# Performance work log

Measured on AMD Instinct MI355X. Metric: run time of the kernel, lower is better.

## Reference

```python
import jax, jax.numpy as jnp
import numpy as np

B, N, C_ATT, H, L = 4, 2048, 256, 8, 2
TOPK = 32        # torch.topk k (only index 0 per channel is used)
NSAMPLE = 32     # max_radius_points
RADIUS = 0.3
EPS = 1e-5


def _bn(x, g, b, axes):
    # training-mode batch norm (biased variance), channel dim = 1
    m = jnp.mean(x, axes, keepdims=True)
    v = jnp.var(x, axes, keepdims=True)
    sh = [1] * x.ndim
    sh[1] = -1
    return (x - m) / jnp.sqrt(v + EPS) * g.reshape(sh) + b.reshape(sh)


def _ln(x, g, b):
    m = jnp.mean(x, -1, keepdims=True)
    v = jnp.var(x, -1, keepdims=True)
    return (x - m) / jnp.sqrt(v + EPS) * g + b


def setup_inputs() -> dict:
    key = jax.random.key(0)
    ks = iter(jax.random.split(key, 40))
    def w(shape, fan):
        return jax.random.normal(next(ks), shape, jnp.float32) / np.sqrt(fan)
    return {
        "hoch_features": jax.random.normal(next(ks), (B, C_ATT, N), jnp.float32),
        "pts": jax.random.uniform(next(ks), (B, 3, N), jnp.float32),
        "Wq": w((L, C_ATT, C_ATT), C_ATT), "Wk": w((L, C_ATT, C_ATT), C_ATT),
        "Wv": w((L, C_ATT, C_ATT), C_ATT), "Wo": w((L, C_ATT, C_ATT), C_ATT),
        "ln_g": jnp.ones((L, C_ATT)), "ln_b": jnp.zeros((L, C_ATT)),
        "fg_w1": w((64, C_ATT), C_ATT), "fg_b1": jnp.zeros((64,)),
        "fg_w2": w((32, 64), 64), "fg_b2": jnp.zeros((32,)),
        "fg_w3": w((16, 32), 32), "fg_b3": jnp.zeros((16,)),
        "fg_g1": jnp.ones((64,)), "fg_be1": jnp.zeros((64,)),
        "fg_g2": jnp.ones((32,)), "fg_be2": jnp.zeros((32,)),
        "fg_g3": jnp.ones((16,)), "fg_be3": jnp.zeros((16,)),
        "cw1": w((64, 3), 3), "cw2": w((256, 64), 64), "cw3": w((512, 256), 256),
        "cg1": jnp.ones((64,)), "cb1": jnp.zeros((64,)),
        "cg2": jnp.ones((256,)), "cb2": jnp.zeros((256,)),
        "cg3": jnp.ones((512,)), "cb3": jnp.zeros((512,)),
    }


def _forward(hoch_features, pts, Wq, Wk, Wv, Wo, ln_g, ln_b,
             fg_w1, fg_b1, fg_w2, fg_b2, fg_w3, fg_b3,
             fg_g1, fg_be1, fg_g2, fg_be2, fg_g3, fg_be3,
             cw1, cw2, cw3, cg1, cb1, cg2, cb2, cg3, cb3):
    # ---- multi-head self-attention stack on (B,N,C) ----
    x = hoch_features.transpose(0, 2, 1)
    dh = C_ATT // H
    for l in range(L):
        q = (x @ Wq[l]).reshape(B, N, H, dh)
        k = (x @ Wk[l]).reshape(B, N, H, dh)
        v = (x @ Wv[l]).reshape(B, N, H, dh)
        att = jax.nn.softmax(jnp.einsum('bnhd,bmhd->bhnm', q, k) / np.sqrt(dh).astype(np.float32))
        o = jnp.einsum('bhnm,bmhd->bnhd', att, v).reshape(B, N, C_ATT) @ Wo[l]
        x = _ln(x + o, ln_g[l], ln_b[l])
    feats = x.transpose(0, 2, 1)                      # (B,256,N)
    # ---- feat_generator: 1x1 conv1d -> BN -> relu chain 256->64->32->16 ----
    h = jax.nn.relu(_bn(jnp.einsum('oc,bcn->bon', fg_w1, feats) + fg_b1[:, None], fg_g1, fg_be1, (0, 2)))
    h = jax.nn.relu(_bn(jnp.einsum('oc,bcn->bon', fg_w2, h) + fg_b2[:, None], fg_g2, fg_be2, (0, 2)))
    h = jax.nn.relu(_bn(jnp.einsum('oc,bcn->bon', fg_w3, h) + fg_b3[:, None], fg_g3, fg_be3, (0, 2)))  # (B,16,N)
    # ---- topk over points, keep argmax per channel -> 16 query points ----
    _, ti = jax.lax.top_k(h, TOPK)                    # (B,16,32)
    idx = ti[:, :, 0]                                 # (B,16)
    all_pts = pts.transpose(0, 2, 1)                  # (B,N,3)
    qpts = jax.vmap(lambda p, i: p[i])(all_pts, idx)  # (B,16,3)
    # ---- ball query (fixed-radius kNN fill, PointNet++ style) ----
    sqd = (jnp.sum(qpts * qpts, -1)[:, :, None] + jnp.sum(all_pts * all_pts, -1)[:, None, :]
           - 2.0 * jnp.einsum('bsc,bnc->bsn', qpts, all_pts))      # (B,16,N)
    gi = jnp.broadcast_to(jnp.arange(N), sqd.shape)
    gi = jnp.where(sqd > RADIUS * RADIUS, N, gi)
    gi = jnp.sort(gi, axis=-1)[:, :, :NSAMPLE]
    gi = jnp.where(gi == N, gi[:, :, :1], gi)         # (B,16,32)
    rpts = jax.vmap(lambda p, i: p[i])(all_pts, gi)   # (B,16,32,3)
    grouped = jnp.concatenate([qpts[:, :, None, :], rpts], axis=2)  # (B,16,33,3)
    g = grouped.transpose(0, 3, 1, 2)                 # (B,3,16,33)
    # ---- 1x1 conv2d -> BN2d -> LeakyReLU(0.2) chain 3->64->256->512 ----
    lrelu = lambda t: jnp.where(t > 0, t, 0.2 * t)
    g = lrelu(_bn(jnp.einsum('oc,bcsk->bosk', cw1, g), cg1, cb1, (0, 2, 3)))
    g = lrelu(_bn(jnp.einsum('oc,bcsk->bosk', cw2, g), cg2, cb2, (0, 2, 3)))
    g = lrelu(_bn(jnp.einsum('oc,bcsk->bosk', cw3, g), cg3, cb3, (0, 2, 3)))
    return jnp.max(g, axis=-1)                        # (B,512,16)


def reference(hoch_features, pts, Wq, Wk, Wv, Wo, ln_g, ln_b,
              fg_w1, fg_b1, fg_w2, fg_b2, fg_w3, fg_b3,
              fg_g1, fg_be1, fg_g2, fg_be2, fg_g3, fg_be3,
              cw1, cw2, cw3, cg1, cb1, cg2, cb2, cg3, cb3):
    return _forward(hoch_features, pts, Wq, Wk, Wv, Wo, ln_g, ln_b,
                    fg_w1, fg_b1, fg_w2, fg_b2, fg_w3, fg_b3,
                    fg_g1, fg_be1, fg_g2, fg_be2, fg_g3, fg_be3,
                    cw1, cw2, cw3, cg1, cb1, cg2, cb2, cg3, cb3)
```

## Files before the change

### kernel.cpp

```cpp
#include <hip/hip_runtime.h>
#include <hip/hip_bf16.h>
#include <math.h>

#define BB 4
#define NN 2048
#define CC 256
#define HH 8
#define DH 32
#define LL 2
#define SS 16
#define KK 33
#define NSAMPLE 32
#define EPSV 1e-5f

typedef _Float16 f16x8 __attribute__((ext_vector_type(8)));
typedef _Float16 f16x4 __attribute__((ext_vector_type(4)));
typedef float f32x4 __attribute__((ext_vector_type(4)));

struct hl16 { _Float16 h, l; };
__device__ __forceinline__ hl16 split2(float v) {
    hl16 r;
    r.h = (_Float16)v;
    r.l = (_Float16)(v - (float)r.h);
    return r;
}

#define INV_MF (1.f / 8192.f)
#define INV_MG (1.f / 2112.f)

#define WT_SLOT 65536
#define FG1H_OFF 1048576
#define FG1L_OFF (FG1H_OFF + 16384)
#define CW2H_OFF (FG1H_OFF + 32768)
#define CW2L_OFF (FG1H_OFF + 49152)
#define CW3H_OFF (FG1H_OFF + 65536)
#define CW3L_OFF (CW3H_OFF + 131072)

__global__ __launch_bounds__(256) void prep_split_k(
    const float* __restrict__ Wq, const float* __restrict__ Wk,
    const float* __restrict__ Wv, const float* __restrict__ Wo,
    const float* __restrict__ fgw1, const float* __restrict__ cw2,
    const float* __restrict__ cw3, _Float16* __restrict__ wt,
    float* __restrict__ stats0) {
    int e = blockIdx.x * 256 + threadIdx.x;
    if (e < 6144) stats0[e] = 0.f;
    if (e < 524288) {
        int slot = e >> 16;
        int l = slot >> 2, mat = slot & 3;
        int r = e & 65535;
        int n = r >> 8, k = r & 255;
        const float* W = mat == 0 ? Wq : mat == 1 ? Wk : mat == 2 ? Wv : Wo;
        hl16 s = split2(W[(size_t)l * 65536 + k * 256 + n]);
        wt[(size_t)(2 * slot) * WT_SLOT + n * 256 + k] = s.h;
        wt[(size_t)(2 * slot + 1) * WT_SLOT + n * 256 + k] = s.l;
    } else if (e < 524288 + 16384) {
        int r = e - 524288;
        hl16 s = split2(fgw1[r]);
        wt[FG1H_OFF + r] = s.h;
        wt[FG1L_OFF + r] = s.l;
    } else if (e < 524288 + 32768) {
        int r = e - (524288 + 16384);
        hl16 s = split2(cw2[r]);
        wt[CW2H_OFF + r] = s.h;
        wt[CW2L_OFF + r] = s.l;
    } else if (e < 524288 + 32768 + 131072) {
        int r = e - (524288 + 32768);
        hl16 s = split2(cw3[r]);
        wt[CW3H_OFF + r] = s.h;
        wt[CW3L_OFF + r] = s.l;
    }
}

__global__ __launch_bounds__(256) void transpose_split_k(const float* __restrict__ in,
                                                         float* __restrict__ out,
                                                         _Float16* __restrict__ oh,
                                                         _Float16* __restrict__ ol) {
    __shared__ float tls[32][33];
    int n0 = blockIdx.x * 32, c0 = blockIdx.y * 32, b = blockIdx.z;
    const float* ip = in + (size_t)b * CC * NN;
    size_t ob = (size_t)b * NN * CC;
    int tx = threadIdx.x, ty = threadIdx.y;
#pragma unroll
    for (int i = 0; i < 4; ++i)
        tls[ty + i * 8][tx] = ip[(size_t)(c0 + ty + i * 8) * NN + n0 + tx];
    __syncthreads();
#pragma unroll
    for (int i = 0; i < 4; ++i) {
        size_t oi = ob + (size_t)(n0 + ty + i * 8) * CC + c0 + tx;
        float v = tls[tx][ty + i * 8];
        out[oi] = v;
        hl16 s = split2(v);
        oh[oi] = s.h;
        ol[oi] = s.l;
    }
}

template <bool TRANSB, bool BIAS>
__global__ __launch_bounds__(256) void gemm_k(const float* __restrict__ A,
                                              const float* __restrict__ Bm,
                                              const float* __restrict__ bias,
                                              float* __restrict__ Cm,
                                              int M, int Nc, int K,
                                              const float* __restrict__ pst,
                                              const float* __restrict__ pg,
                                              const float* __restrict__ pb,
                                              float pInvM,
                                              float* __restrict__ ost) {
    __shared__ float As[16][68];
    __shared__ float Bs[16][68];
    __shared__ float sSc[64], sSh[64];
    int t = threadIdx.x;
    int tx = t & 15, ty = t >> 4;
    int row0 = blockIdx.y * 64, col0 = blockIdx.x * 64;
    if (pst && t < K) {
        float mean = pst[t] * pInvM;
        float var = pst[K + t] * pInvM - mean * mean;
        float wv = rsqrtf(var + EPSV) * pg[t];
        sSc[t] = wv;
        sSh[t] = pb[t] - mean * wv;
    }
    if (pst) __syncthreads();
    float acc[4][4] = {};
    for (int k0 = 0; k0 < K; k0 += 16) {
#pragma unroll
        for (int p = 0; p < 4; ++p) {
            int i = t + 256 * p;
            int m = i >> 4, k = i & 15;
            int gm = row0 + m, gk = k0 + k;
            float av = 0.f;
            if (gm < M && gk < K) {
                av = A[(size_t)gm * K + gk];
                if (pst) {
                    av = fmaf(av, sSc[gk], sSh[gk]);
                    av = fmaxf(av, 0.f);
                }
            }
            As[k][m] = av;
        }
#pragma unroll
        for (int p = 0; p < 4; ++p) {
            int i = t + 256 * p;
            if (TRANSB) {
                int k = i & 15, n = i >> 4;
                int gn = col0 + n, gk = k0 + k;
                Bs[k][n] = (gn < Nc && gk < K) ? Bm[(size_t)gn * K + gk] : 0.f;
            } else {
                int n = i & 63, k = i >> 6;
                int gn = col0 + n, gk = k0 + k;
                Bs[k][n] = (gn < Nc && gk < K) ? Bm[(size_t)gk * Nc + gn] : 0.f;
            }
        }
        __syncthreads();
#pragma unroll
        for (int kk = 0; kk < 16; ++kk) {
            float4 a4 = *(const float4*)&As[kk][ty * 4];
            float4 b4 = *(const float4*)&Bs[kk][tx * 4];
            float av[4] = {a4.x, a4.y, a4.z, a4.w};
            float bv[4] = {b4.x, b4.y, b4.z, b4.w};
#pragma unroll
            for (int i = 0; i < 4; ++i)
#pragma unroll
                for (int j = 0; j < 4; ++j) acc[i][j] = fmaf(av[i], bv[j], acc[i][j]);
        }
        __syncthreads();
    }
    float cs[4] = {}, css[4] = {};
#pragma unroll
    for (int i = 0; i < 4; ++i) {
        int r = row0 + ty * 4 + i;
        if (r >= M) continue;
#pragma unroll
        for (int j = 0; j < 4; ++j) {
            int c = col0 + tx * 4 + j;
            if (c >= Nc) continue;
            float v = acc[i][j];
            if (BIAS) v += bias[c];
            Cm[(size_t)r * Nc + c] = v;
            cs[j] += v;
            css[j] += v * v;
        }
    }
    if (ost) {
        float* sc = &As[0][0];
        if (t < 128) sc[t] = 0.f;
        __syncthreads();
#pragma unroll
        for (int j = 0; j < 4; ++j) {
            atomicAdd(&sc[tx * 4 + j], cs[j]);
            atomicAdd(&sc[64 + tx * 4 + j], css[j]);
        }
        __syncthreads();
        if (t < Nc) atomicAdd(&ost[t], sc[t]);
        else if (t >= 64 && t - 64 < Nc) atomicAdd(&ost[Nc + t - 64], sc[t]);
    }
}

#define EPI_F32 0
#define EPI_QK 1
#define EPI_VT 2

template <int TM>
__device__ __forceinline__ void gemm_h_body(
    const _Float16* __restrict__ Ah, const _Float16* __restrict__ Al,
    const _Float16* __restrict__ Bh, const _Float16* __restrict__ Bl,
    const float* __restrict__ bias, float* __restrict__ Cf,
    _Float16* __restrict__ Ch, _Float16* __restrict__ Cl,
    int Nc, int K, int row0, int col0, int mode, float scl,
    float* __restrict__ ost,
    _Float16* sAh, _Float16* sAl, _Float16* sBh, _Float16* sBl) {
    int t = threadIdx.x, w = t >> 6, lane = t & 63;
    int col = lane & 15, quad = lane >> 4;
    const int m0w = (TM == 128) ? (w & 1) * 64 : 0;
    const int n0w = (TM == 128) ? (w >> 1) * 32 : w * 16;
    constexpr int NT = (TM == 128) ? 2 : 1;
    constexpr int AC = TM / 64;
    f32x4 acc[4][NT];
#pragma unroll
    for (int i = 0; i < 4; ++i)
#pragma unroll
        for (int j = 0; j < NT; ++j) acc[i][j] = (f32x4){0.f, 0.f, 0.f, 0.f};

    for (int k0 = 0; k0 < K; k0 += 32) {
        f16x8 rah[AC], ral[AC], rbh, rbl;
#pragma unroll
        for (int i = 0; i < AC; ++i) {
            int idx = t + 256 * i;
            int r = idx >> 2, off = (idx & 3) * 8;
            rah[i] = *(const f16x8*)(Ah + (size_t)(row0 + r) * K + k0 + off);
            ral[i] = *(const f16x8*)(Al + (size_t)(row0 + r) * K + k0 + off);
        }
        {
            int r = t >> 2, off = (t & 3) * 8;
            rbh = *(const f16x8*)(Bh + (size_t)(col0 + r) * K + k0 + off);
            rbl = *(const f16x8*)(Bl + (size_t)(col0 + r) * K + k0 + off);
        }
        __syncthreads();
#pragma unroll
        for (int i = 0; i < AC; ++i) {
            int idx = t + 256 * i;
            int r = idx >> 2, off = (idx & 3) * 8;
            *(f16x8*)&sAh[r * 40 + off] = rah[i];
            *(f16x8*)&sAl[r * 40 + off] = ral[i];
        }
        {
            int r = t >> 2, off = (t & 3) * 8;
            *(f16x8*)&sBh[r * 40 + off] = rbh;
            *(f16x8*)&sBl[r * 40 + off] = rbl;
        }
        __syncthreads();
        f16x8 fah[4], fal[4], fbh[NT], fbl[NT];
#pragma unroll
        for (int i = 0; i < 4; ++i) {
            fah[i] = *(const f16x8*)&sAh[(m0w + i * 16 + col) * 40 + quad * 8];
            fal[i] = *(const f16x8*)&sAl[(m0w + i * 16 + col) * 40 + quad * 8];
        }
#pragma unroll
        for (int j = 0; j < NT; ++j) {
            fbh[j] = *(const f16x8*)&sBh[(n0w + j * 16 + col) * 40 + quad * 8];
            fbl[j] = *(const f16x8*)&sBl[(n0w + j * 16 + col) * 40 + quad * 8];
        }
#pragma unroll
        for (int i = 0; i < 4; ++i)
#pragma unroll
            for (int j = 0; j < NT; ++j) {
                acc[i][j] = __builtin_amdgcn_mfma_f32_16x16x32_f16(fah[i], fbh[j], acc[i][j], 0, 0, 0);
                acc[i][j] = __builtin_amdgcn_mfma_f32_16x16x32_f16(fah[i], fbl[j], acc[i][j], 0, 0, 0);
                acc[i][j] = __builtin_amdgcn_mfma_f32_16x16x32_f16(fal[i], fbh[j], acc[i][j], 0, 0, 0);
            }
    }
    float s = 0.f, ss = 0.f;
#pragma unroll
    for (int i = 0; i < 4; ++i)
#pragma unroll
        for (int j = 0; j < NT; ++j) {
            int n = col0 + n0w + j * 16 + col;
            int mb = row0 + m0w + i * 16 + quad * 4;
            if (mode == EPI_F32) {
                float bv = bias ? bias[n] : 0.f;
#pragma unroll
                for (int r = 0; r < 4; ++r) {
                    float v = acc[i][j][r] + bv;
                    Cf[(size_t)(mb + r) * Nc + n] = v;
                    s += v;
                    ss += v * v;
                }
            } else if (mode == EPI_QK) {
#pragma unroll
                for (int r = 0; r < 4; ++r) {
                    hl16 sp = split2(acc[i][j][r] * scl);
                    Ch[(size_t)(mb + r) * Nc + n] = sp.h;
                    Cl[(size_t)(mb + r) * Nc + n] = sp.l;
                }
            } else {
                int b = mb >> 11, token = mb & 2047;
                int h = n >> 5, d = n & 31;
                f16x4 h4, l4;
#pragma unroll
                for (int r = 0; r < 4; ++r) {
                    hl16 sp = split2(acc[i][j][r]);
                    h4[r] = sp.h;
                    l4[r] = sp.l;
                }
                size_t dst = ((size_t)(b * HH + h) * DH + d) * NN + token;
                *(f16x4*)&Ch[dst] = h4;
                *(f16x4*)&Cl[dst] = l4;
            }
        }
    if (ost && mode == EPI_F32 && TM == 64) {
        s += __shfl_xor(s, 16);
        s += __shfl_xor(s, 32);
        ss += __shfl_xor(ss, 16);
        ss += __shfl_xor(ss, 32);
        if (quad == 0) {
            int n = col0 + n0w + col;
            atomicAdd(&ost[n], s);
            atomicAdd(&ost[Nc + n], ss);
        }
    }
}

template <int TM>
__global__ __launch_bounds__(256) void gemm_h_k(const _Float16* __restrict__ Ah,
                                                const _Float16* __restrict__ Al,
                                                const _Float16* __restrict__ Bh,
                                                const _Float16* __restrict__ Bl,
                                                const float* __restrict__ bias,
                                                float* __restrict__ Cf, int Nc, int K,
                                                float* __restrict__ ost) {
    __shared__ _Float16 sAh[TM * 40], sAl[TM * 40], sBh[64 * 40], sBl[64 * 40];
    gemm_h_body<TM>(Ah, Al, Bh, Bl, bias, Cf, nullptr, nullptr, Nc, K,
                    blockIdx.y * TM, blockIdx.x * 64, EPI_F32, 1.f, ost,
                    sAh, sAl, sBh, sBl);
}

__global__ __launch_bounds__(256) void qkv_h_k(const _Float16* __restrict__ Xh,
                                               const _Float16* __restrict__ Xl,
                                               const _Float16* __restrict__ wt, int layer,
                                               _Float16* Qh, _Float16* Ql,
                                               _Float16* Kh, _Float16* Kl,
                                               _Float16* Vh, _Float16* Vl) {
    __shared__ _Float16 sAh[128 * 40], sAl[128 * 40], sBh[64 * 40], sBl[64 * 40];
    int mat = blockIdx.x >> 2;
    int slot = (layer * 4 + mat) * 2;
    const _Float16* Bh = wt + (size_t)slot * WT_SLOT;
    const _Float16* Bl = wt + (size_t)(slot + 1) * WT_SLOT;
    _Float16* Ch = mat == 0 ? Qh : mat == 1 ? Kh : Vh;
    _Float16* Cl = mat == 0 ? Ql : mat == 1 ? Kl : Vl;
    int mode = (mat == 2) ? EPI_VT : EPI_QK;
    float scl = (mat == 0) ? 0.25501654859214384f : 1.f;
    gemm_h_body<128>(Xh, Xl, Bh, Bl, nullptr, nullptr, Ch, Cl, CC, CC,
                     blockIdx.y * 128, (blockIdx.x & 3) * 64, mode, scl, nullptr,
                     sAh, sAl, sBh, sBl);
}

__global__ __launch_bounds__(256) void attn5_k(_Float16* QOh, _Float16* QOl,
                                               const _Float16* __restrict__ Kh,
                                               const _Float16* __restrict__ Kl,
                                               const _Float16* __restrict__ Vh,
                                               const _Float16* __restrict__ Vl) {
    __shared__ _Float16 sKh[64 * 40], sKl[64 * 40];
    __shared__ _Float16 sVh[32 * 72], sVl[32 * 72];
    __shared__ _Float16 sPh[4][16 * 40], sPl[4][16 * 40];
    int t = threadIdx.x, w = t >> 6, lane = t & 63;
    int col = lane & 15, quad = lane >> 4;
    int bh = blockIdx.y, b = bh >> 3, h = bh & 7;
    int qbase = blockIdx.x * 64 + w * 16;

    size_t qoff = ((size_t)(b * NN + qbase + col)) * CC + h * DH + quad * 8;
    f16x8 qh = *(const f16x8*)(QOh + qoff);
    f16x8 ql = *(const f16x8*)(QOl + qoff);

    f32x4 o0 = {0.f, 0.f, 0.f, 0.f}, o1 = {0.f, 0.f, 0.f, 0.f};
    float mrun = -1e30f, lsum = 0.f;

    const _Float16* fKh = &sKh[col * 40 + quad * 8];
    const _Float16* fKl = &sKl[col * 40 + quad * 8];
    const _Float16* fVh0 = &sVh[col * 72 + quad * 8];
    const _Float16* fVl0 = &sVl[col * 72 + quad * 8];
    const _Float16* fVh1 = &sVh[(16 + col) * 72 + quad * 8];
    const _Float16* fVl1 = &sVl[(16 + col) * 72 + quad * 8];
    _Float16* wPh = &sPh[w][col * 40 + quad * 4];
    _Float16* wPl = &sPl[w][col * 40 + quad * 4];
    const _Float16* rPh = &sPh[w][col * 40 + quad * 8];
    const _Float16* rPl = &sPl[w][col * 40 + quad * 8];

    int pidx = t & 127;
    int krow = pidx >> 1, koff = (pidx & 1) * 16;
    int vrow = pidx >> 2, voff = (pidx & 3) * 16;
    const _Float16* kg = (t < 128 ? Kh : Kl) + (size_t)b * NN * CC + h * DH;
    const _Float16* vg = (t < 128 ? Vh : Vl) + ((size_t)(b * HH + h) * DH + vrow) * NN;
    _Float16* dK = (t < 128 ? sKh : sKl) + krow * 40 + koff;
    _Float16* dV = (t < 128 ? sVh : sVl) + vrow * 72 + voff;

    for (int k0 = 0; k0 < NN; k0 += 64) {
        const _Float16* kp = kg + (size_t)(k0 + krow) * CC + koff;
        f16x8 rk0 = *(const f16x8*)kp;
        f16x8 rk1 = *(const f16x8*)(kp + 8);
        const _Float16* vp = vg + k0 + voff;
        f16x8 rv0 = *(const f16x8*)vp;
        f16x8 rv1 = *(const f16x8*)(vp + 8);
        __syncthreads();
        *(f16x8*)dK = rk0;
        *(f16x8*)(dK + 8) = rk1;
        *(f16x8*)dV = rv0;
        *(f16x8*)(dV + 8) = rv1;
        __syncthreads();

        f32x4 s[4];
#pragma unroll
        for (int kt = 0; kt < 4; ++kt) {
            f16x8 ka = *(const f16x8*)(fKh + kt * 16 * 40);
            f16x8 kb = *(const f16x8*)(fKl + kt * 16 * 40);
            f32x4 z = {0.f, 0.f, 0.f, 0.f};
            z = __builtin_amdgcn_mfma_f32_16x16x32_f16(ka, qh, z, 0, 0, 0);
            z = __builtin_amdgcn_mfma_f32_16x16x32_f16(ka, ql, z, 0, 0, 0);
            z = __builtin_amdgcn_mfma_f32_16x16x32_f16(kb, qh, z, 0, 0, 0);
            s[kt] = z;
        }

        float tm = -1e30f;
#pragma unroll
        for (int kt = 0; kt < 4; ++kt)
#pragma unroll
            for (int r = 0; r < 4; ++r) tm = fmaxf(tm, s[kt][r]);
        tm = fmaxf(tm, __shfl_xor(tm, 16));
        tm = fmaxf(tm, __shfl_xor(tm, 32));
        float nm = fmaxf(mrun, tm);
        float alpha = __builtin_amdgcn_exp2f(mrun - nm);
        float p[16], rs = 0.f;
#pragma unroll
        for (int kt = 0; kt < 4; ++kt)
#pragma unroll
            for (int r = 0; r < 4; ++r) {
                float pv = __builtin_amdgcn_exp2f(s[kt][r] - nm);
                p[kt * 4 + r] = pv;
                rs += pv;
            }
        rs += __shfl_xor(rs, 16);
        rs += __shfl_xor(rs, 32);
        lsum = lsum * alpha + rs;
        mrun = nm;
        o0.x *= alpha; o0.y *= alpha; o0.z *= alpha; o0.w *= alpha;
        o1.x *= alpha; o1.y *= alpha; o1.z *= alpha; o1.w *= alpha;

#pragma unroll
        for (int c = 0; c < 2; ++c) {
#pragma unroll
            for (int k2 = 0; k2 < 2; ++k2) {
                int kt = c * 2 + k2;
                f16x4 h4, l4;
#pragma unroll
                for (int r = 0; r < 4; ++r) {
                    hl16 sp = split2(p[kt * 4 + r]);
                    h4[r] = sp.h;
                    l4[r] = sp.l;
                }
                *(f16x4*)(wPh + k2 * 16) = h4;
                *(f16x4*)(wPl + k2 * 16) = l4;
            }
            __asm__ volatile("s_waitcnt lgkmcnt(0)" ::: "memory");
            f16x8 pH = *(const f16x8*)rPh;
            f16x8 pL = *(const f16x8*)rPl;

            f16x8 va = *(const f16x8*)(fVh0 + c * 32);
            f16x8 vb = *(const f16x8*)(fVl0 + c * 32);
            o0 = __builtin_amdgcn_mfma_f32_16x16x32_f16(va, pH, o0, 0, 0, 0);
            o0 = __builtin_amdgcn_mfma_f32_16x16x32_f16(va, pL, o0, 0, 0, 0);
            o0 = __builtin_amdgcn_mfma_f32_16x16x32_f16(vb, pH, o0, 0, 0, 0);
            f16x8 vc = *(const f16x8*)(fVh1 + c * 32);
            f16x8 vd = *(const f16x8*)(fVl1 + c * 32);
            o1 = __builtin_amdgcn_mfma_f32_16x16x32_f16(vc, pH, o1, 0, 0, 0);
            o1 = __builtin_amdgcn_mfma_f32_16x16x32_f16(vc, pL, o1, 0, 0, 0);
            o1 = __builtin_amdgcn_mfma_f32_16x16x32_f16(vd, pH, o1, 0, 0, 0);
        }
    }

    float inv = 1.f / lsum;
    f32x4 oo[2] = {o0, o1};
#pragma unroll
    for (int dh = 0; dh < 2; ++dh) {
        f16x4 h4, l4;
#pragma unroll
        for (int r = 0; r < 4; ++r) {
            hl16 s = split2(oo[dh][r] * inv);
            h4[r] = s.h;
            l4[r] = s.l;
        }
        size_t dsti = ((size_t)(b * NN + qbase + col)) * CC + h * DH + dh * 16 + quad * 4;
        *(f16x4*)&QOh[dsti] = h4;
        *(f16x4*)&QOl[dsti] = l4;
    }
}

__global__ __launch_bounds__(256) void add_ln_k(float* __restrict__ X,
                                                const float* __restrict__ P,
                                                const float* __restrict__ g,
                                                const float* __restrict__ bta,
                                                _Float16* __restrict__ Xh,
                                                _Float16* __restrict__ Xl) {
    int wave = threadIdx.x >> 6, lane = threadIdx.x & 63;
    size_t row = (size_t)blockIdx.x * 4 + wave;
    size_t base = row * CC + lane * 4;
    float4 x = *(float4*)(X + base);
    float4 p = *(const float4*)(P + base);
    x.x += p.x; x.y += p.y; x.z += p.z; x.w += p.w;
    float sum = x.x + x.y + x.z + x.w;
    float ss = x.x * x.x + x.y * x.y + x.z * x.z + x.w * x.w;
#pragma unroll
    for (int off = 32; off; off >>= 1) {
        sum += __shfl_down(sum, off);
        ss += __shfl_down(ss, off);
    }
    sum = __shfl(sum, 0);
    ss = __shfl(ss, 0);
    float mean = sum * (1.f / 256.f);
    float var = ss * (1.f / 256.f) - mean * mean;
    float wn = rsqrtf(var + EPSV);
    float4 gg = *(const float4*)(g + lane * 4);
    float4 bb = *(const float4*)(bta + lane * 4);
    x.x = (x.x - mean) * wn * gg.x + bb.x;
    x.y = (x.y - mean) * wn * gg.y + bb.y;
    x.z = (x.z - mean) * wn * gg.z + bb.z;
    x.w = (x.w - mean) * wn * gg.w + bb.w;
    *(float4*)(X + base) = x;
    f16x4 h4, l4;
    float xv[4] = {x.x, x.y, x.z, x.w};
#pragma unroll
    for (int j = 0; j < 4; ++j) {
        hl16 s = split2(xv[j]);
        h4[j] = s.h;
        l4[j] = s.l;
    }
    *(f16x4*)&Xh[base] = h4;
    *(f16x4*)&Xl[base] = l4;
}

__global__ __launch_bounds__(256) void applyc_k(const float* __restrict__ in,
                                                _Float16* __restrict__ oh,
                                                _Float16* __restrict__ ol,
                                                const float* __restrict__ st,
                                                const float* __restrict__ gam,
                                                const float* __restrict__ bet,
                                                int total, int Cc, float invM) {
    int i = blockIdx.x * 256 + threadIdx.x;
    if (i >= total) return;
    int c = i % Cc;
    float mean = st[c] * invM;
    float var = st[Cc + c] * invM - mean * mean;
    float sc = rsqrtf(var + EPSV) * gam[c];
    float v = fmaf(in[i] - mean, sc, bet[c]);
    v = v > 0.f ? v : 0.2f * v;
    hl16 s = split2(v);
    oh[i] = s.h;
    ol[i] = s.l;
}

__global__ __launch_bounds__(64) void select_k(const float* __restrict__ H3,
                                               const float* __restrict__ pts,
                                               const float* __restrict__ st,
                                               const float* __restrict__ gam,
                                               const float* __restrict__ bet,
                                               float* __restrict__ G0) {
    int bs = blockIdx.x;
    int b = bs >> 4, ch = bs & 15;
    int lane = threadIdx.x;
    float mean = st[ch] * INV_MF;
    float var = st[16 + ch] * INV_MF - mean * mean;
    float sc = rsqrtf(var + EPSV) * gam[ch];
    float sh = bet[ch] - mean * sc;
    float best = -1e30f;
    int bn = 0;
    for (int n = lane; n < NN; n += 64) {
        float v = fmaf(H3[((size_t)(b * NN + n)) * 16 + ch], sc, sh);
        v = fmaxf(v, 0.f);
        if (v > best) { best = v; bn = n; }
    }
#pragma unroll
    for (int off = 32; off; off >>= 1) {
        float ov = __shfl_xor(best, off);
        int on = __shfl_xor(bn, off);
        if (ov > best || (ov == best && on < bn)) { best = ov; bn = on; }
    }
    const float* px = pts + (size_t)b * 3 * NN;
    float qx = px[bn], qy = px[NN + bn], qz = px[2 * NN + bn];
    float qq = (qx * qx + qy * qy) + qz * qz;
    __shared__ int sgi[NSAMPLE];
    const float R2 = 0.09f;
    int cnt = 0;
    for (int base = 0; base < NN && cnt < NSAMPLE; base += 64) {
        int n = base + lane;
        float x = px[n], y = px[NN + n], z = px[2 * NN + n];
        float pp = (x * x + y * y) + z * z;
        float dot = (qx * x + qy * y) + qz * z;
        float sqd = (qq + pp) - 2.f * dot;
        bool ok = !(sqd > R2);
        unsigned long long mk = __ballot(ok);
        int pos = cnt + (int)__popcll(mk & ((1ull << lane) - 1ull));
        if (ok && pos < NSAMPLE) sgi[pos] = n;
        cnt += (int)__popcll(mk);
    }
    __syncthreads();
    int g0 = sgi[0];
    if (lane >= cnt && lane < NSAMPLE) sgi[lane] = g0;
    __syncthreads();
    for (int e = lane; e < KK * 3; e += 64) {
        int k = e / 3, d = e % 3;
        int src = (k == 0) ? bn : sgi[k - 1];
        G0[((size_t)bs * KK + k) * 3 + d] = px[d * NN + src];
    }
}

__global__ __launch_bounds__(256) void maxpool_k(const float* __restrict__ G3,
                                                 const float* __restrict__ st,
                                                 const float* __restrict__ gam,
                                                 const float* __restrict__ bet,
                                                 float* __restrict__ out) {
    int i = blockIdx.x * 256 + threadIdx.x;
    if (i >= BB * 512 * SS) return;
    int o = i & 511;
    int s = (i >> 9) & 15;
    int b = i >> 13;
    float mean = st[o] * INV_MG;
    float var = st[512 + o] * INV_MG - mean * mean;
    float sc = rsqrtf(var + EPSV) * gam[o];
    float sh = bet[o] - mean * sc;
    const float* p = G3 + ((size_t)(b * SS + s) * KK) * 512 + o;
    float mx = -1e30f;
#pragma unroll
    for (int k = 0; k < KK; ++k) {
        float v = fmaf(p[(size_t)k * 512], sc, sh);
        v = v > 0.f ? v : 0.2f * v;
        mx = fmaxf(mx, v);
    }
    out[((size_t)(b * 512 + o)) * SS + s] = mx;
}

extern "C" void kernel_launch(void* const* d_in, const int* in_sizes, int n_in,
                              void* d_out, int out_size, void* d_ws, size_t ws_size,
                              hipStream_t stream) {
    const float* hoch = (const float*)d_in[0];
    const float* pts = (const float*)d_in[1];
    const float* Wq = (const float*)d_in[2];
    const float* Wk = (const float*)d_in[3];
    const float* Wv = (const float*)d_in[4];
    const float* Wo = (const float*)d_in[5];
    const float* ln_g = (const float*)d_in[6];
    const float* ln_b = (const float*)d_in[7];
    const float* fg_w1 = (const float*)d_in[8];
    const float* fg_b1 = (const float*)d_in[9];
    const float* fg_w2 = (const float*)d_in[10];
    const float* fg_b2 = (const float*)d_in[11];
    const float* fg_w3 = (const float*)d_in[12];
    const float* fg_b3 = (const float*)d_in[13];
    const float* fg_g1 = (const float*)d_in[14];
    const float* fg_be1 = (const float*)d_in[15];
    const float* fg_g2 = (const float*)d_in[16];
    const float* fg_be2 = (const float*)d_in[17];
    const float* fg_g3 = (const float*)d_in[18];
    const float* fg_be3 = (const float*)d_in[19];
    const float* cw1 = (const float*)d_in[20];
    const float* cw2 = (const float*)d_in[21];
    const float* cw3 = (const float*)d_in[22];
    const float* cg1 = (const float*)d_in[23];
    const float* cb1 = (const float*)d_in[24];
    const float* cg2 = (const float*)d_in[25];
    const float* cb2 = (const float*)d_in[26];
    const float* cg3 = (const float*)d_in[27];
    const float* cb3 = (const float*)d_in[28];
    float* out = (float*)d_out;

    float* ws = (float*)d_ws;
    const size_t M1 = (size_t)BB * NN * CC;
    float* X = ws;
    float* bA = ws + M1;
    float* bB = ws + 2 * M1;
    float* bC = ws + 3 * M1;
    _Float16* hb = (_Float16*)(ws + 4 * M1);
    _Float16* Xh = hb;
    _Float16* Xl = hb + M1;
    _Float16* Qh = hb + 2 * M1;
    _Float16* Ql = hb + 3 * M1;
    _Float16* Kh = hb + 4 * M1;
    _Float16* Kl = hb + 5 * M1;
    _Float16* Vh = hb + 6 * M1;
    _Float16* Vl = hb + 7 * M1;
    _Float16* wt = hb + 8 * M1;
    float* sm = ws + 4 * M1 + (9 * M1) / 2;
    float* st1 = sm;
    float* st2 = sm + 1024;
    float* st3 = sm + 2048;
    float* st4 = sm + 3072;
    float* st5 = sm + 4096;
    float* st6 = sm + 5120;
    float* G0 = sm + 8192;

    prep_split_k<<<2688, 256, 0, stream>>>(Wq, Wk, Wv, Wo, fg_w1, cw2, cw3, wt, sm);
    transpose_split_k<<<dim3(NN / 32, CC / 32, BB), dim3(32, 8), 0, stream>>>(hoch, X, Xh, Xl);

    const int Mrows = BB * NN;
    for (int l = 0; l < LL; ++l) {
        qkv_h_k<<<dim3(12, Mrows / 128), 256, 0, stream>>>(Xh, Xl, wt, l, Qh, Ql, Kh, Kl, Vh, Vl);
        attn5_k<<<dim3(NN / 64, BB * HH), 256, 0, stream>>>(Qh, Ql, Kh, Kl, Vh, Vl);
        int slot = (l * 4 + 3) * 2;
        gemm_h_k<128><<<dim3(CC / 64, Mrows / 128), 256, 0, stream>>>(
            Qh, Ql, wt + (size_t)slot * WT_SLOT, wt + (size_t)(slot + 1) * WT_SLOT,
            nullptr, bA, CC, CC, nullptr);
        add_ln_k<<<Mrows / 4, 256, 0, stream>>>(X, bA, ln_g + l * CC, ln_b + l * CC, Xh, Xl);
    }

    gemm_h_k<64><<<dim3(1, Mrows / 64), 256, 0, stream>>>(Xh, Xl, wt + FG1H_OFF, wt + FG1L_OFF, fg_b1, bA, 64, 256, st1);
    gemm_k<true, true><<<dim3(1, Mrows / 64), 256, 0, stream>>>(bA, fg_w2, fg_b2, bB, Mrows, 32, 64,
                                                                st1, fg_g1, fg_be1, INV_MF, st2);
    gemm_k<true, true><<<dim3(1, Mrows / 64), 256, 0, stream>>>(bB, fg_w3, fg_b3, bC, Mrows, 16, 32,
                                                                st2, fg_g2, fg_be2, INV_MF, st3);

    select_k<<<BB * SS, 64, 0, stream>>>(bC, pts, st3, fg_g3, fg_be3, G0);

    const int Mg = BB * SS * KK;
    gemm_k<true, false><<<dim3(1, Mg / 64), 256, 0, stream>>>(G0, cw1, nullptr, bA, Mg, 64, 3,
                                                              nullptr, nullptr, nullptr, 0.f, st4);
    applyc_k<<<(Mg * 64 + 255) / 256, 256, 0, stream>>>(bA, Kh, Kl, st4, cg1, cb1, Mg * 64, 64, INV_MG);
    gemm_h_k<64><<<dim3(4, Mg / 64), 256, 0, stream>>>(Kh, Kl, wt + CW2H_OFF, wt + CW2L_OFF, nullptr, bB, 256, 64, st5);
    applyc_k<<<(Mg * 256 + 255) / 256, 256, 0, stream>>>(bB, Kh, Kl, st5, cg2, cb2, Mg * 256, 256, INV_MG);
    gemm_h_k<64><<<dim3(8, Mg / 64), 256, 0, stream>>>(Kh, Kl, wt + CW3H_OFF, wt + CW3L_OFF, nullptr, bC, 512, 256, st6);

    maxpool_k<<<(BB * 512 * SS + 255) / 256, 256, 0, stream>>>(bC, st6, cg3, cb3, out);

    (void)in_sizes; (void)n_in; (void)out_size; (void)ws_size;
}
```

Before: 466.9 us.

## Split attention over two key halves and merge partials in a combine kernel

The attention kernel now splits the key sequence into two halves along a new grid dimension, so twice as many blocks run. Each block writes unnormalized fp32 partial outputs plus its running max and sum. A new combine kernel rescales the two partials by their log-sum-exp weights, normalizes them, and writes the split fp16 hi/lo output. This raises occupancy on a grid of 1024 blocks at the cost of an extra launch and extra fp32 global traffic for the partial results.

```diff
diff --git a/kernel.cpp b/kernel.cpp
--- a/kernel.cpp
+++ b/kernel.cpp
@@ -353,22 +353,27 @@
                      sAh, sAl, sBh, sBl);
 }
 
-__global__ __launch_bounds__(256) void attn5_k(_Float16* QOh, _Float16* QOl,
+__global__ __launch_bounds__(256) void attn6_k(const _Float16* __restrict__ Qhp,
+                                               const _Float16* __restrict__ Qlp,
                                                const _Float16* __restrict__ Kh,
                                                const _Float16* __restrict__ Kl,
                                                const _Float16* __restrict__ Vh,
-                                               const _Float16* __restrict__ Vl) {
+                                               const _Float16* __restrict__ Vl,
+                                               float* __restrict__ O0,
+                                               float* __restrict__ O1,
+                                               float* __restrict__ ML) {
     __shared__ _Float16 sKh[64 * 40], sKl[64 * 40];
     __shared__ _Float16 sVh[32 * 72], sVl[32 * 72];
     __shared__ _Float16 sPh[4][16 * 40], sPl[4][16 * 40];
     int t = threadIdx.x, w = t >> 6, lane = t & 63;
     int col = lane & 15, quad = lane >> 4;
-    int bh = blockIdx.y, b = bh >> 3, h = bh & 7;
+    int bh = blockIdx.z, b = bh >> 3, h = bh & 7;
+    int kh = blockIdx.y;
     int qbase = blockIdx.x * 64 + w * 16;
 
     size_t qoff = ((size_t)(b * NN + qbase + col)) * CC + h * DH + quad * 8;
-    f16x8 qh = *(const f16x8*)(QOh + qoff);
-    f16x8 ql = *(const f16x8*)(QOl + qoff);
+    f16x8 qh = *(const f16x8*)(Qhp + qoff);
+    f16x8 ql = *(const f16x8*)(Qlp + qoff);
 
     f32x4 o0 = {0.f, 0.f, 0.f, 0.f}, o1 = {0.f, 0.f, 0.f, 0.f};
     float mrun = -1e30f, lsum = 0.f;
@@ -392,7 +397,8 @@
     _Float16* dK = (t < 128 ? sKh : sKl) + krow * 40 + koff;
     _Float16* dV = (t < 128 ? sVh : sVl) + vrow * 72 + voff;
 
-    for (int k0 = 0; k0 < NN; k0 += 64) {
+    int kbase = kh * (NN / 2);
+    for (int k0 = kbase; k0 < kbase + NN / 2; k0 += 64) {
         const _Float16* kp = kg + (size_t)(k0 + krow) * CC + koff;
         f16x8 rk0 = *(const f16x8*)kp;
         f16x8 rk1 = *(const f16x8*)(kp + 8);
@@ -475,20 +481,51 @@
         }
     }
 
-    float inv = 1.f / lsum;
-    f32x4 oo[2] = {o0, o1};
-#pragma unroll
-    for (int dh = 0; dh < 2; ++dh) {
+    float* OP = (kh == 0) ? O0 : O1;
+    int q = qbase + col;
+    size_t oi = ((size_t)bh * NN + q) * 32;
+    *(f32x4*)&OP[oi + quad * 4] = o0;
+    *(f32x4*)&OP[oi + 16 + quad * 4] = o1;
+    if (quad == 0) {
+        float2* mlp = (float2*)ML;
+        mlp[(size_t)kh * (BB * HH * NN) + (size_t)bh * NN + q] = make_float2(mrun, lsum);
+    }
+}
+
+__global__ __launch_bounds__(256) void attn_comb_k(const float* __restrict__ O0,
+                                                   const float* __restrict__ O1,
+                                                   const float* __restrict__ ML,
+                                                   _Float16* __restrict__ QOh,
+                                                   _Float16* __restrict__ QOl) {
+    int i = blockIdx.x * 256 + threadIdx.x;
+    int bh = i >> 11, q = i & 2047;
+    int b = bh >> 3, h = bh & 7;
+    const float2* mlp = (const float2*)ML;
+    float2 ml0 = mlp[i];
+    float2 ml1 = mlp[BB * HH * NN + i];
+    float m = fmaxf(ml0.x, ml1.x);
+    float a0 = __builtin_amdgcn_exp2f(ml0.x - m);
+    float a1 = __builtin_amdgcn_exp2f(ml1.x - m);
+    float inv = 1.f / (ml0.y * a0 + ml1.y * a1);
+    a0 *= inv;
+    a1 *= inv;
+    size_t src = (size_t)i * 32;
+    size_t dst = ((size_t)(b * NN + q)) * CC + h * DH;
+#pragma unroll
+    for (int d = 0; d < 32; d += 4) {
+        float4 v0 = *(const float4*)&O0[src + d];
+        float4 v1 = *(const float4*)&O1[src + d];
+        float vv[4] = {v0.x * a0 + v1.x * a1, v0.y * a0 + v1.y * a1,
+                       v0.z * a0 + v1.z * a1, v0.w * a0 + v1.w * a1};
         f16x4 h4, l4;
 #pragma unroll
         for (int r = 0; r < 4; ++r) {
-            hl16 s = split2(oo[dh][r] * inv);
+            hl16 s = split2(vv[r]);
             h4[r] = s.h;
             l4[r] = s.l;
         }
-        size_t dsti = ((size_t)(b * NN + qbase + col)) * CC + h * DH + dh * 16 + quad * 4;
-        *(f16x4*)&QOh[dsti] = h4;
-        *(f16x4*)&QOl[dsti] = l4;
+        *(f16x4*)&QOh[dst + d] = h4;
+        *(f16x4*)&QOl[dst + d] = l4;
     }
 }
 
@@ -700,7 +737,8 @@
     const int Mrows = BB * NN;
     for (int l = 0; l < LL; ++l) {
         qkv_h_k<<<dim3(12, Mrows / 128), 256, 0, stream>>>(Xh, Xl, wt, l, Qh, Ql, Kh, Kl, Vh, Vl);
-        attn5_k<<<dim3(NN / 64, BB * HH), 256, 0, stream>>>(Qh, Ql, Kh, Kl, Vh, Vl);
+        attn6_k<<<dim3(NN / 64, 2, BB * HH), 256, 0, stream>>>(Qh, Ql, Kh, Kl, Vh, Vl, bB, bC, bA);
+        attn_comb_k<<<BB * HH * NN / 256, 256, 0, stream>>>(bB, bC, bA, Qh, Ql);
         int slot = (l * 4 + 3) * 2;
         gemm_h_k<128><<<dim3(CC / 64, Mrows / 128), 256, 0, stream>>>(
             Qh, Ql, wt + (size_t)slot * WT_SLOT, wt + (size_t)(slot + 1) * WT_SLOT,
```

Measured after the change: 477.2 us. 2.2% more time.
